# Performance work log

Measured on AMD Instinct MI355X. Metric: run time of the kernel, lower is better.

## Reference

```python
import jax, jax.numpy as jnp
import numpy as np

TEMPERATURE = 0.07


def _l2norm(x, axis, eps=1e-12):
    n = jnp.sqrt(jnp.sum(x * x, axis=axis, keepdims=True))
    return x / jnp.maximum(n, eps)


def _bilinear_sample(img, x, y):
    # img: (C,H,W); x,y: (N,) pixel coords. Matches F.grid_sample(mode='bilinear',
    # padding_mode='zeros', align_corners=True) after the norm/denorm round trip.
    C, H, W = img.shape
    x0 = jnp.floor(x); y0 = jnp.floor(y)
    x1 = x0 + 1.0;     y1 = y0 + 1.0
    wx1 = x - x0; wx0 = 1.0 - wx1
    wy1 = y - y0; wy0 = 1.0 - wy1

    def gather(xi, yi, w):
        inb = (xi >= 0) & (xi <= W - 1) & (yi >= 0) & (yi <= H - 1)
        xc = jnp.clip(xi, 0, W - 1).astype(jnp.int32)
        yc = jnp.clip(yi, 0, H - 1).astype(jnp.int32)
        v = img[:, yc, xc]  # (C,N)
        return v * (w * inb)[None, :]

    return (gather(x0, y0, wx0 * wy0) + gather(x1, y0, wx1 * wy0)
            + gather(x0, y1, wx0 * wy1) + gather(x1, y1, wx1 * wy1))


def setup_inputs() -> dict:
    key = jax.random.key(0)
    k1, k2, k3, k4 = jax.random.split(key, 4)
    B, C, Hf, Wf = 32, 256, 64, 64
    Ho, Wo = 512, 512
    fmap_rgb = jax.random.normal(k1, (B, C, Hf, Wf), dtype=jnp.float32)
    fmap_depth = jax.random.normal(k2, (B, C, Hf, Wf), dtype=jnp.float32)
    # uniform coords inside the original image so sampled positions are in-range
    projected_coords = jax.random.uniform(k3, (B, 2, Ho, Wo), dtype=jnp.float32) * (Wo - 1)
    valid_mask = jax.random.uniform(k4, (B, 1, Ho, Wo), dtype=jnp.float32)
    return {"fmap_rgb": fmap_rgb, "fmap_depth": fmap_depth,
            "projected_coords": projected_coords, "valid_mask": valid_mask}


def reference(fmap_rgb, fmap_depth, projected_coords, valid_mask):
    B, C, Hf, Wf = fmap_rgb.shape
    Ho = projected_coords.shape[2]
    ds = Ho // Hf

    fr = _l2norm(fmap_rgb, axis=1)
    fd = _l2norm(fmap_depth, axis=1)

    coords_f = projected_coords[:, :, ::ds, ::ds]   # (B,2,Hf,Wf)
    vm_f = valid_mask[:, :, ::ds, ::ds]             # (B,1,Hf,Wf)

    step = max(1, Hf // 16)
    gh, gw = jnp.meshgrid(jnp.arange(0, Hf, step), jnp.arange(0, Wf, step), indexing='ij')
    ghf = gh.reshape(-1); gwf = gw.reshape(-1)
    N = ghf.shape[0]  # num_grid (~256)

    depth_feats = fd[:, :, ghf, gwf]                # (B,C,N)
    rgb_neg = fr[:, :, ghf, gwf]                    # (B,C,N)
    proj_u = coords_f[:, 0, ghf, gwf] / ds          # (B,N) pixel coords in feat space
    proj_v = coords_f[:, 1, ghf, gwf] / ds
    grid_valid = vm_f[:, 0, ghf, gwf] > 0.5         # (B,N)

    # positive features via bilinear sampling (computed in the original; not used
    # in the loss because labels index into rgb_neg, i.e. the diagonal)
    _rgb_pos = jax.vmap(_bilinear_sample)(fr, proj_u, proj_v)  # (B,C,N)

    sim = jnp.einsum('bcn,bcm->bnm', depth_feats, rgb_neg) / TEMPERATURE  # (B,N,N)

    neg_inf = jnp.asarray(-1e30, sim.dtype)
    sim_m = jnp.where(grid_valid[:, None, :], sim, neg_inf)  # mask invalid columns
    logZ = jax.nn.logsumexp(sim_m, axis=-1)                  # (B,N)
    diag = jnp.einsum('bnn->bn', sim)                        # positive logits
    row_loss = logZ - diag                                   # per-row CE

    vf = grid_valid.astype(sim.dtype)
    n_valid = grid_valid.sum(axis=-1)                        # (B,) int
    include = n_valid >= 2                                   # skip batches with <2 valid
    loss_b = (row_loss * vf).sum(axis=-1) / jnp.maximum(n_valid, 1).astype(sim.dtype)
    avg_loss = jnp.where(include, loss_b, 0.0).sum() / B

    preds = jnp.argmax(sim_m, axis=-1)                       # (B,N)
    correct = (preds == jnp.arange(N)[None, :]) & grid_valid & include[:, None]
    total_count = jnp.where(include, n_valid, 0).sum()
    accuracy = jnp.where(total_count > 0,
                         correct.sum().astype(sim.dtype) /
                         jnp.maximum(total_count, 1).astype(sim.dtype) * 100.0,
                         0.0)
    avg_loss = jnp.where(total_count > 0, avg_loss, 0.0)
    return avg_loss, accuracy
```

## Files before the change

### kernel.cpp

```cpp
#include <hip/hip_runtime.h>
#include <math.h>

#define BB   32
#define CC   256
#define HF   64
#define WF   64
#define NN   256
#define MROWS 32
#define NSTRIP (NN / MROWS)
#define SIMP 260
#define NXCD 8

typedef __attribute__((ext_vector_type(8))) short    bf16x8;
typedef __attribute__((ext_vector_type(4))) float    f32x4;
typedef __attribute__((ext_vector_type(8))) unsigned short u16x8;

__device__ inline unsigned short f2bf(float f) {
    unsigned u = __float_as_uint(f);
    unsigned r = u + 0x7FFFu + ((u >> 16) & 1u);
    return (unsigned short)(r >> 16);
}

__global__ __launch_bounds__(256) void gather_kernel(
        const float* __restrict__ fr,
        const float* __restrict__ fd,
        const float* __restrict__ vm,
        unsigned short* __restrict__ Dbf,
        unsigned short* __restrict__ Rbf,
        float* __restrict__ nPartD,
        float* __restrict__ nPartR,
        float* __restrict__ GV) {
    __shared__ float ldsD[16][257];
    __shared__ float ldsR[16][257];

    int blk = blockIdx.x;
    int xcd = blk & (NXCD - 1);
    int r   = blk >> 3;
    int b   = xcd * 4 + (r & 3);
    int i   = r >> 2;
    int t   = threadIdx.x;

    size_t base = ((size_t)(b * CC + t) * HF + 4 * i) * WF;
#pragma unroll
    for (int j = 0; j < 16; ++j) {
        ldsD[j][t] = fd[base + 4 * j];
        ldsR[j][t] = fr[base + 4 * j];
    }
    __syncthreads();

    int j = t >> 4, p = t & 15;
    float vd_[16], vr_[16];
    float ssd = 0.0f, ssr = 0.0f;
#pragma unroll
    for (int q = 0; q < 16; ++q) {
        float a = ldsD[j][p * 16 + q];
        float c2 = ldsR[j][p * 16 + q];
        vd_[q] = a; vr_[q] = c2;
        ssd = fmaf(a, a, ssd);
        ssr = fmaf(c2, c2, ssr);
    }
    int n = i * 16 + j;
    nPartD[(size_t)(b * 16 + p) * NN + n] = ssd;
    nPartR[(size_t)(b * 16 + p) * NN + n] = ssr;

    unsigned short db[16], rb[16];
#pragma unroll
    for (int q = 0; q < 16; ++q) { db[q] = f2bf(vd_[q]); rb[q] = f2bf(vr_[q]); }
    unsigned short* dDst = Dbf + ((size_t)(b * NN + n) * CC + p * 16);
    unsigned short* rDst = Rbf + ((size_t)(b * NN + n) * CC + p * 16);
    *reinterpret_cast<u16x8*>(dDst)     = *reinterpret_cast<u16x8*>(&db[0]);
    *reinterpret_cast<u16x8*>(dDst + 8) = *reinterpret_cast<u16x8*>(&db[8]);
    *reinterpret_cast<u16x8*>(rDst)     = *reinterpret_cast<u16x8*>(&rb[0]);
    *reinterpret_cast<u16x8*>(rDst + 8) = *reinterpret_cast<u16x8*>(&rb[8]);

    if (t < 16) {
        float v = vm[((size_t)b * 512 + 32 * i) * 512 + 32 * t];
        GV[(size_t)b * NN + i * 16 + t] = (v > 0.5f) ? 1.0f : 0.0f;
    }
}

__global__ __launch_bounds__(256) void sim_loss_kernel(
        const unsigned short* __restrict__ Dbf,
        const unsigned short* __restrict__ Rbf,
        const float* __restrict__ nPartD,
        const float* __restrict__ nPartR,
        const float* __restrict__ GV,
        float* __restrict__ lossPart,
        float* __restrict__ corrPart) {
    __shared__ float simLds[MROWS * SIMP];
    __shared__ float colInv[NN];
    __shared__ float validF[NN];
    __shared__ float rowInv[MROWS];
    __shared__ float diagLds[MROWS];
    __shared__ float rowLoss[MROWS];
    __shared__ float rowCorr[MROWS];

    int blk   = blockIdx.x;
    int xcd   = blk & (NXCD - 1);
    int rr    = blk >> 3;
    int b     = xcd * 4 + (rr & 3);
    int strip = rr >> 2;
    int nbase = strip * MROWS;

    int t  = threadIdx.x;
    int w  = t >> 6;
    int l  = t & 63;
    int lg = l >> 4, lr = l & 15;

    {
        float ss = 0.0f;
#pragma unroll
        for (int p = 0; p < 16; ++p) ss += nPartR[(size_t)(b * 16 + p) * NN + t];
        colInv[t] = 1.0f / fmaxf(sqrtf(ss), 1e-12f);
        validF[t] = GV[(size_t)b * NN + t];
    }
    if (t < MROWS) {
        float ss = 0.0f;
#pragma unroll
        for (int p = 0; p < 16; ++p) ss += nPartD[(size_t)(b * 16 + p) * NN + nbase + t];
        rowInv[t] = 1.0f / fmaxf(sqrtf(ss), 1e-12f);
    }
    __syncthreads();

    const unsigned short* Dp = Dbf + (size_t)(b * NN + nbase) * CC;
    const unsigned short* Rp = Rbf + (size_t)b * NN * CC;

    f32x4 acc[2][4] = {};

#pragma unroll
    for (int ks = 0; ks < 8; ++ks) {
        int coff = ks * 32 + lg * 8;
        bf16x8 a0 = *reinterpret_cast<const bf16x8*>(Dp + (size_t)(lr)      * CC + coff);
        bf16x8 a1 = *reinterpret_cast<const bf16x8*>(Dp + (size_t)(16 + lr) * CC + coff);
        bf16x8 b0 = *reinterpret_cast<const bf16x8*>(Rp + (size_t)(w * 64 +  0 + lr) * CC + coff);
        bf16x8 b1 = *reinterpret_cast<const bf16x8*>(Rp + (size_t)(w * 64 + 16 + lr) * CC + coff);
        bf16x8 b2 = *reinterpret_cast<const bf16x8*>(Rp + (size_t)(w * 64 + 32 + lr) * CC + coff);
        bf16x8 b3 = *reinterpret_cast<const bf16x8*>(Rp + (size_t)(w * 64 + 48 + lr) * CC + coff);
        acc[0][0] = __builtin_amdgcn_mfma_f32_16x16x32_bf16(a0, b0, acc[0][0], 0, 0, 0);
        acc[0][1] = __builtin_amdgcn_mfma_f32_16x16x32_bf16(a0, b1, acc[0][1], 0, 0, 0);
        acc[0][2] = __builtin_amdgcn_mfma_f32_16x16x32_bf16(a0, b2, acc[0][2], 0, 0, 0);
        acc[0][3] = __builtin_amdgcn_mfma_f32_16x16x32_bf16(a0, b3, acc[0][3], 0, 0, 0);
        acc[1][0] = __builtin_amdgcn_mfma_f32_16x16x32_bf16(a1, b0, acc[1][0], 0, 0, 0);
        acc[1][1] = __builtin_amdgcn_mfma_f32_16x16x32_bf16(a1, b1, acc[1][1], 0, 0, 0);
        acc[1][2] = __builtin_amdgcn_mfma_f32_16x16x32_bf16(a1, b2, acc[1][2], 0, 0, 0);
        acc[1][3] = __builtin_amdgcn_mfma_f32_16x16x32_bf16(a1, b3, acc[1][3], 0, 0, 0);
    }

    const float invT = 1.0f / 0.07f;
#pragma unroll
    for (int mi = 0; mi < 2; ++mi) {
#pragma unroll
        for (int ni = 0; ni < 4; ++ni) {
            int col = w * 64 + ni * 16 + lr;
            float ci = colInv[col];
            float gv = validF[col];
#pragma unroll
            for (int reg = 0; reg < 4; ++reg) {
                int lrow = mi * 16 + lg * 4 + reg;
                float s = acc[mi][ni][reg] * invT * rowInv[lrow] * ci;
                if (col == nbase + lrow) diagLds[lrow] = s;
                simLds[lrow * SIMP + col] = (gv > 0.5f) ? s : -1e30f;
            }
        }
    }
    __syncthreads();

    for (int k = w; k < MROWS; k += 4) {
        const float* row = &simLds[k * SIMP];
        float v0 = row[l];
        float v1 = row[64 + l];
        float v2 = row[128 + l];
        float v3 = row[192 + l];
        float mv = v0; int mi = l;
        if (v1 > mv) { mv = v1; mi = l + 64; }
        if (v2 > mv) { mv = v2; mi = l + 128; }
        if (v3 > mv) { mv = v3; mi = l + 192; }
#pragma unroll
        for (int off = 32; off > 0; off >>= 1) {
            float ov = __shfl_xor(mv, off, 64);
            int   oi = __shfl_xor(mi, off, 64);
            if (ov > mv || (ov == mv && oi < mi)) { mv = ov; mi = oi; }
        }
        float e = __expf(v0 - mv) + __expf(v1 - mv) + __expf(v2 - mv) + __expf(v3 - mv);
#pragma unroll
        for (int off = 32; off > 0; off >>= 1) e += __shfl_xor(e, off, 64);
        if (l == 0) {
            float vfn = validF[nbase + k];
            float lz = mv + __logf(e);
            rowLoss[k] = (vfn > 0.5f) ? (lz - diagLds[k]) : 0.0f;
            rowCorr[k] = (vfn > 0.5f && mi == nbase + k) ? 1.0f : 0.0f;
        }
    }
    __syncthreads();

    if (t == 0) {
        float la = 0.0f, ca = 0.0f;
#pragma unroll
        for (int k = 0; k < MROWS; ++k) { la += rowLoss[k]; ca += rowCorr[k]; }
        lossPart[(size_t)b * NSTRIP + strip] = la;
        corrPart[(size_t)b * NSTRIP + strip] = ca;
    }
}

__global__ __launch_bounds__(256) void finalize_kernel(
        const float* __restrict__ GV,
        const float* __restrict__ lossPart,
        const float* __restrict__ corrPart,
        float* __restrict__ out) {
    __shared__ float sl[BB], sc2[BB], st2[BB];
    int t = threadIdx.x;
    int b = t >> 3, s = t & 7;

    float nvp = 0.0f;
    const float4* g4 = reinterpret_cast<const float4*>(GV + (size_t)b * NN);
#pragma unroll
    for (int q = 0; q < 8; ++q) {
        float4 v = g4[s * 8 + q];
        nvp += v.x + v.y + v.z + v.w;
    }
#pragma unroll
    for (int off = 1; off < 8; off <<= 1) nvp += __shfl_xor(nvp, off, 64);

    if (s == 0) {
        float lb = 0.0f, cb = 0.0f;
#pragma unroll
        for (int k = 0; k < NSTRIP; ++k) {
            lb += lossPart[b * NSTRIP + k];
            cb += corrPart[b * NSTRIP + k];
        }
        bool inc = (nvp >= 2.0f);
        sl[b]  = inc ? (lb / fmaxf(nvp, 1.0f)) : 0.0f;
        sc2[b] = inc ? cb : 0.0f;
        st2[b] = inc ? nvp : 0.0f;
    }
    __syncthreads();
    if (t == 0) {
        float L = 0.0f, Ccnt = 0.0f, Tcnt = 0.0f;
        for (int bb = 0; bb < BB; ++bb) { L += sl[bb]; Ccnt += sc2[bb]; Tcnt += st2[bb]; }
        float avg = L / (float)BB;
        out[0] = (Tcnt > 0.0f) ? avg : 0.0f;
        out[1] = (Tcnt > 0.0f) ? (Ccnt / fmaxf(Tcnt, 1.0f) * 100.0f) : 0.0f;
    }
}

extern "C" void kernel_launch(void* const* d_in, const int* in_sizes, int n_in,
                              void* d_out, int out_size, void* d_ws, size_t ws_size,
                              hipStream_t stream) {
    const float* fr = (const float*)d_in[0];
    const float* fd = (const float*)d_in[1];
    const float* vm = (const float*)d_in[3];

    float* out = (float*)d_out;
    char* ws = (char*)d_ws;

    size_t featBytes = (size_t)BB * NN * CC * 2;
    size_t partBytes = (size_t)BB * 16 * NN * 4;
    unsigned short* Dbf = (unsigned short*)ws;
    unsigned short* Rbf = (unsigned short*)(ws + featBytes);
    float* nPartD   = (float*)(ws + 2 * featBytes);
    float* nPartR   = (float*)(ws + 2 * featBytes + partBytes);
    float* GV       = (float*)(ws + 2 * featBytes + 2 * partBytes);
    float* lossPart = GV + (size_t)BB * NN;
    float* corrPart = lossPart + BB * NSTRIP;

    hipLaunchKernelGGL(gather_kernel, dim3(BB * 16), dim3(256), 0, stream,
                       fr, fd, vm, Dbf, Rbf, nPartD, nPartR, GV);
    hipLaunchKernelGGL(sim_loss_kernel, dim3(BB * NSTRIP), dim3(256), 0, stream,
                       Dbf, Rbf, nPartD, nPartR, GV, lossPart, corrPart);
    hipLaunchKernelGGL(finalize_kernel, dim3(1), dim3(256), 0, stream,
                       GV, lossPart, corrPart, out);
}
```

Measured before the change: 40.31 us.

## Fuse gather, similarity-loss and finalize kernels into one cooperative kernel with grid sync

Combines the three launches into a single cooperative kernel of 256 blocks of 512 threads, with grid.sync between the gather, similarity/loss and final-reduction phases. This removes two kernel launches and their inter-kernel gaps. Each block now handles two gather tiles and one similarity strip with 8 waves, each wave covering 32 columns instead of 64. The risks are the cost of the grid-wide barriers, the larger LDS footprint (about 66KB), which limits occupancy, and a single block doing the final reduction.

```diff
diff --git a/kernel.cpp b/kernel.cpp
--- a/kernel.cpp
+++ b/kernel.cpp
@@ -1,5 +1,8 @@
 #include <hip/hip_runtime.h>
+#include <hip/hip_cooperative_groups.h>
 #include <math.h>
+
+namespace cg = cooperative_groups;
 
 #define BB   32
 #define CC   256
@@ -10,6 +13,7 @@
 #define NSTRIP (NN / MROWS)
 #define SIMP 260
 #define NXCD 8
+#define GBLK 256
 
 typedef __attribute__((ext_vector_type(8))) short    bf16x8;
 typedef __attribute__((ext_vector_type(4))) float    f32x4;
@@ -21,7 +25,7 @@
     return (unsigned short)(r >> 16);
 }
 
-__global__ __launch_bounds__(256) void gather_kernel(
+__global__ __launch_bounds__(512) void fused_kernel(
         const float* __restrict__ fr,
         const float* __restrict__ fd,
         const float* __restrict__ vm,
@@ -29,64 +33,14 @@
         unsigned short* __restrict__ Rbf,
         float* __restrict__ nPartD,
         float* __restrict__ nPartR,
-        float* __restrict__ GV) {
-    __shared__ float ldsD[16][257];
-    __shared__ float ldsR[16][257];
-
-    int blk = blockIdx.x;
-    int xcd = blk & (NXCD - 1);
-    int r   = blk >> 3;
-    int b   = xcd * 4 + (r & 3);
-    int i   = r >> 2;
-    int t   = threadIdx.x;
-
-    size_t base = ((size_t)(b * CC + t) * HF + 4 * i) * WF;
-#pragma unroll
-    for (int j = 0; j < 16; ++j) {
-        ldsD[j][t] = fd[base + 4 * j];
-        ldsR[j][t] = fr[base + 4 * j];
-    }
-    __syncthreads();
-
-    int j = t >> 4, p = t & 15;
-    float vd_[16], vr_[16];
-    float ssd = 0.0f, ssr = 0.0f;
-#pragma unroll
-    for (int q = 0; q < 16; ++q) {
-        float a = ldsD[j][p * 16 + q];
-        float c2 = ldsR[j][p * 16 + q];
-        vd_[q] = a; vr_[q] = c2;
-        ssd = fmaf(a, a, ssd);
-        ssr = fmaf(c2, c2, ssr);
-    }
-    int n = i * 16 + j;
-    nPartD[(size_t)(b * 16 + p) * NN + n] = ssd;
-    nPartR[(size_t)(b * 16 + p) * NN + n] = ssr;
-
-    unsigned short db[16], rb[16];
-#pragma unroll
-    for (int q = 0; q < 16; ++q) { db[q] = f2bf(vd_[q]); rb[q] = f2bf(vr_[q]); }
-    unsigned short* dDst = Dbf + ((size_t)(b * NN + n) * CC + p * 16);
-    unsigned short* rDst = Rbf + ((size_t)(b * NN + n) * CC + p * 16);
-    *reinterpret_cast<u16x8*>(dDst)     = *reinterpret_cast<u16x8*>(&db[0]);
-    *reinterpret_cast<u16x8*>(dDst + 8) = *reinterpret_cast<u16x8*>(&db[8]);
-    *reinterpret_cast<u16x8*>(rDst)     = *reinterpret_cast<u16x8*>(&rb[0]);
-    *reinterpret_cast<u16x8*>(rDst + 8) = *reinterpret_cast<u16x8*>(&rb[8]);
-
-    if (t < 16) {
-        float v = vm[((size_t)b * 512 + 32 * i) * 512 + 32 * t];
-        GV[(size_t)b * NN + i * 16 + t] = (v > 0.5f) ? 1.0f : 0.0f;
-    }
-}
-
-__global__ __launch_bounds__(256) void sim_loss_kernel(
-        const unsigned short* __restrict__ Dbf,
-        const unsigned short* __restrict__ Rbf,
-        const float* __restrict__ nPartD,
-        const float* __restrict__ nPartR,
-        const float* __restrict__ GV,
+        float* __restrict__ GV,
         float* __restrict__ lossPart,
-        float* __restrict__ corrPart) {
+        float* __restrict__ corrPart,
+        float* __restrict__ out) {
+    cg::grid_group grid = cg::this_grid();
+
+    __shared__ float gD[2][16][257];
+    __shared__ float gR[2][16][257];
     __shared__ float simLds[MROWS * SIMP];
     __shared__ float colInv[NN];
     __shared__ float validF[NN];
@@ -94,20 +48,68 @@
     __shared__ float diagLds[MROWS];
     __shared__ float rowLoss[MROWS];
     __shared__ float rowCorr[MROWS];
-
-    int blk   = blockIdx.x;
-    int xcd   = blk & (NXCD - 1);
-    int rr    = blk >> 3;
-    int b     = xcd * 4 + (rr & 3);
-    int strip = rr >> 2;
+    __shared__ float sl[BB], sc2[BB], st2[BB];
+
+    int blk = blockIdx.x;
+    int t   = threadIdx.x;
+    int xcd = blk & (NXCD - 1);
+    int q   = blk >> 3;
+
+    {
+        int half = t >> 8;
+        int tt   = t & 255;
+        int ul   = q * 2 + half;
+        int gb   = xcd * 4 + (ul & 3);
+        int gi   = ul >> 2;
+
+        size_t base = ((size_t)(gb * CC + tt) * HF + 4 * gi) * WF;
+#pragma unroll
+        for (int j = 0; j < 16; ++j) {
+            gD[half][j][tt] = fd[base + 4 * j];
+            gR[half][j][tt] = fr[base + 4 * j];
+        }
+        __syncthreads();
+
+        int j = tt >> 4, p = tt & 15;
+        float ssd = 0.0f, ssr = 0.0f;
+        unsigned short db[16], rb[16];
+#pragma unroll
+        for (int c2 = 0; c2 < 16; ++c2) {
+            float a = gD[half][j][p * 16 + c2];
+            float c = gR[half][j][p * 16 + c2];
+            db[c2] = f2bf(a);
+            rb[c2] = f2bf(c);
+            ssd = fmaf(a, a, ssd);
+            ssr = fmaf(c, c, ssr);
+        }
+        int n = gi * 16 + j;
+        nPartD[(size_t)(gb * 16 + p) * NN + n] = ssd;
+        nPartR[(size_t)(gb * 16 + p) * NN + n] = ssr;
+
+        unsigned short* dDst = Dbf + ((size_t)(gb * NN + n) * CC + p * 16);
+        unsigned short* rDst = Rbf + ((size_t)(gb * NN + n) * CC + p * 16);
+        *reinterpret_cast<u16x8*>(dDst)     = *reinterpret_cast<u16x8*>(&db[0]);
+        *reinterpret_cast<u16x8*>(dDst + 8) = *reinterpret_cast<u16x8*>(&db[8]);
+        *reinterpret_cast<u16x8*>(rDst)     = *reinterpret_cast<u16x8*>(&rb[0]);
+        *reinterpret_cast<u16x8*>(rDst + 8) = *reinterpret_cast<u16x8*>(&rb[8]);
+
+        if (tt < 16) {
+            float v = vm[((size_t)gb * 512 + 32 * gi) * 512 + 32 * tt];
+            GV[(size_t)gb * NN + gi * 16 + tt] = (v > 0.5f) ? 1.0f : 0.0f;
+        }
+    }
+
+    grid.sync();
+
+    int b     = xcd * 4 + (q & 3);
+    int strip = q >> 2;
     int nbase = strip * MROWS;
 
-    int t  = threadIdx.x;
     int w  = t >> 6;
     int l  = t & 63;
     int lg = l >> 4, lr = l & 15;
 
-    {
+    if (t < NN) {
         float ss = 0.0f;
 #pragma unroll
         for (int p = 0; p < 16; ++p) ss += nPartR[(size_t)(b * 16 + p) * NN + t];
@@ -123,35 +125,29 @@
     __syncthreads();
 
     const unsigned short* Dp = Dbf + (size_t)(b * NN + nbase) * CC;
-    const unsigned short* Rp = Rbf + (size_t)b * NN * CC;
-
-    f32x4 acc[2][4] = {};
+    const unsigned short* Rp = Rbf + (size_t)(b * NN + w * 32) * CC;
+
+    f32x4 acc[2][2] = {};
 
 #pragma unroll
     for (int ks = 0; ks < 8; ++ks) {
         int coff = ks * 32 + lg * 8;
         bf16x8 a0 = *reinterpret_cast<const bf16x8*>(Dp + (size_t)(lr)      * CC + coff);
         bf16x8 a1 = *reinterpret_cast<const bf16x8*>(Dp + (size_t)(16 + lr) * CC + coff);
-        bf16x8 b0 = *reinterpret_cast<const bf16x8*>(Rp + (size_t)(w * 64 +  0 + lr) * CC + coff);
-        bf16x8 b1 = *reinterpret_cast<const bf16x8*>(Rp + (size_t)(w * 64 + 16 + lr) * CC + coff);
-        bf16x8 b2 = *reinterpret_cast<const bf16x8*>(Rp + (size_t)(w * 64 + 32 + lr) * CC + coff);
-        bf16x8 b3 = *reinterpret_cast<const bf16x8*>(Rp + (size_t)(w * 64 + 48 + lr) * CC + coff);
+        bf16x8 b0 = *reinterpret_cast<const bf16x8*>(Rp + (size_t)(lr)      * CC + coff);
+        bf16x8 b1 = *reinterpret_cast<const bf16x8*>(Rp + (size_t)(16 + lr) * CC + coff);
         acc[0][0] = __builtin_amdgcn_mfma_f32_16x16x32_bf16(a0, b0, acc[0][0], 0, 0, 0);
         acc[0][1] = __builtin_amdgcn_mfma_f32_16x16x32_bf16(a0, b1, acc[0][1], 0, 0, 0);
-        acc[0][2] = __builtin_amdgcn_mfma_f32_16x16x32_bf16(a0, b2, acc[0][2], 0, 0, 0);
-        acc[0][3] = __builtin_amdgcn_mfma_f32_16x16x32_bf16(a0, b3, acc[0][3], 0, 0, 0);
         acc[1][0] = __builtin_amdgcn_mfma_f32_16x16x32_bf16(a1, b0, acc[1][0], 0, 0, 0);
         acc[1][1] = __builtin_amdgcn_mfma_f32_16x16x32_bf16(a1, b1, acc[1][1], 0, 0, 0);
-        acc[1][2] = __builtin_amdgcn_mfma_f32_16x16x32_bf16(a1, b2, acc[1][2], 0, 0, 0);
-        acc[1][3] = __builtin_amdgcn_mfma_f32_16x16x32_bf16(a1, b3, acc[1][3], 0, 0, 0);
     }
 
     const float invT = 1.0f / 0.07f;
 #pragma unroll
     for (int mi = 0; mi < 2; ++mi) {
 #pragma unroll
-        for (int ni = 0; ni < 4; ++ni) {
-            int col = w * 64 + ni * 16 + lr;
+        for (int ni = 0; ni < 2; ++ni) {
+            int col = w * 32 + ni * 16 + lr;
             float ci = colInv[col];
             float gv = validF[col];
 #pragma unroll
@@ -165,7 +161,7 @@
     }
     __syncthreads();
 
-    for (int k = w; k < MROWS; k += 4) {
+    for (int k = w; k < MROWS; k += 8) {
         const float* row = &simLds[k * SIMP];
         float v0 = row[l];
         float v1 = row[64 + l];
@@ -200,46 +196,43 @@
         lossPart[(size_t)b * NSTRIP + strip] = la;
         corrPart[(size_t)b * NSTRIP + strip] = ca;
     }
-}
-
-__global__ __launch_bounds__(256) void finalize_kernel(
-        const float* __restrict__ GV,
-        const float* __restrict__ lossPart,
-        const float* __restrict__ corrPart,
-        float* __restrict__ out) {
-    __shared__ float sl[BB], sc2[BB], st2[BB];
-    int t = threadIdx.x;
-    int b = t >> 3, s = t & 7;
-
-    float nvp = 0.0f;
-    const float4* g4 = reinterpret_cast<const float4*>(GV + (size_t)b * NN);
-#pragma unroll
-    for (int q = 0; q < 8; ++q) {
-        float4 v = g4[s * 8 + q];
-        nvp += v.x + v.y + v.z + v.w;
-    }
-#pragma unroll
-    for (int off = 1; off < 8; off <<= 1) nvp += __shfl_xor(nvp, off, 64);
-
-    if (s == 0) {
-        float lb = 0.0f, cb = 0.0f;
-#pragma unroll
-        for (int k = 0; k < NSTRIP; ++k) {
-            lb += lossPart[b * NSTRIP + k];
-            cb += corrPart[b * NSTRIP + k];
-        }
-        bool inc = (nvp >= 2.0f);
-        sl[b]  = inc ? (lb / fmaxf(nvp, 1.0f)) : 0.0f;
-        sc2[b] = inc ? cb : 0.0f;
-        st2[b] = inc ? nvp : 0.0f;
-    }
-    __syncthreads();
-    if (t == 0) {
-        float L = 0.0f, Ccnt = 0.0f, Tcnt = 0.0f;
-        for (int bb = 0; bb < BB; ++bb) { L += sl[bb]; Ccnt += sc2[bb]; Tcnt += st2[bb]; }
-        float avg = L / (float)BB;
-        out[0] = (Tcnt > 0.0f) ? avg : 0.0f;
-        out[1] = (Tcnt > 0.0f) ? (Ccnt / fmaxf(Tcnt, 1.0f) * 100.0f) : 0.0f;
+
+    grid.sync();
+
+    if (blk == 0) {
+        int bb = t >> 3, s = t & 7;
+        if (t < 256) {
+            float nvp = 0.0f;
+            const float4* g4 = reinterpret_cast<const float4*>(GV + (size_t)bb * NN);
+#pragma unroll
+            for (int qq = 0; qq < 8; ++qq) {
+                float4 v = g4[s * 8 + qq];
+                nvp += v.x + v.y + v.z + v.w;
+            }
+#pragma unroll
+            for (int off = 1; off < 8; off <<= 1) nvp += __shfl_xor(nvp, off, 64);
+
+            if (s == 0) {
+                float lb = 0.0f, cb = 0.0f;
+#pragma unroll
+                for (int k = 0; k < NSTRIP; ++k) {
+                    lb += lossPart[bb * NSTRIP + k];
+                    cb += corrPart[bb * NSTRIP + k];
+                }
+                bool inc = (nvp >= 2.0f);
+                sl[bb]  = inc ? (lb / fmaxf(nvp, 1.0f)) : 0.0f;
+                sc2[bb] = inc ? cb : 0.0f;
+                st2[bb] = inc ? nvp : 0.0f;
+            }
+        }
+        __syncthreads();
+        if (t == 0) {
+            float L = 0.0f, Ccnt = 0.0f, Tcnt = 0.0f;
+            for (int qq = 0; qq < BB; ++qq) { L += sl[qq]; Ccnt += sc2[qq]; Tcnt += st2[qq]; }
+            float avg = L / (float)BB;
+            out[0] = (Tcnt > 0.0f) ? avg : 0.0f;
+            out[1] = (Tcnt > 0.0f) ? (Ccnt / fmaxf(Tcnt, 1.0f) * 100.0f) : 0.0f;
+        }
     }
 }
 
@@ -250,7 +243,7 @@
     const float* fd = (const float*)d_in[1];
     const float* vm = (const float*)d_in[3];
 
-    float* out = (float*)d_out;
+    float* outp = (float*)d_out;
     char* ws = (char*)d_ws;
 
     size_t featBytes = (size_t)BB * NN * CC * 2;
@@ -263,10 +256,11 @@
     float* lossPart = GV + (size_t)BB * NN;
     float* corrPart = lossPart + BB * NSTRIP;
 
-    hipLaunchKernelGGL(gather_kernel, dim3(BB * 16), dim3(256), 0, stream,
-                       fr, fd, vm, Dbf, Rbf, nPartD, nPartR, GV);
-    hipLaunchKernelGGL(sim_loss_kernel, dim3(BB * NSTRIP), dim3(256), 0, stream,
-                       Dbf, Rbf, nPartD, nPartR, GV, lossPart, corrPart);
-    hipLaunchKernelGGL(finalize_kernel, dim3(1), dim3(256), 0, stream,
-                       GV, lossPart, corrPart, out);
+    void* args[] = {
+        (void*)&fr, (void*)&fd, (void*)&vm,
+        (void*)&Dbf, (void*)&Rbf, (void*)&nPartD, (void*)&nPartR,
+        (void*)&GV, (void*)&lossPart, (void*)&corrPart, (void*)&outp
+    };
+    hipLaunchCooperativeKernel((void*)fused_kernel, dim3(GBLK), dim3(512),
+                               args, 0, stream);
 }
```

Measured after the change: 111.6 us. 2.77x slower.
